# Kernel tuning notes

Measured on AMD Instinct MI355X. Metric: run time of the kernel, lower is better.

Reference implementation:

```python
import jax, jax.numpy as jnp
import numpy as np

B = 131072   # batch
D = 64       # latent_dim
P = 32       # n_pairs
H = 64       # hidden_dim
EMA = 1.0    # ema buffer initial value (detached in original, so a constant)


def setup_inputs() -> dict:
    key = jax.random.key(0)
    ks = jax.random.split(key, 4)
    z = jax.random.normal(ks[0], (B, D), dtype=jnp.float32)
    # tiny MLP params (2 -> H -> H -> 1), small init so exp(score) stays finite
    W1 = jax.random.normal(ks[1], (2, H), dtype=jnp.float32) * 0.05
    b1 = jnp.zeros((H,), jnp.float32)
    W2 = jax.random.normal(ks[2], (H, H), dtype=jnp.float32) * 0.05
    b2 = jnp.zeros((H,), jnp.float32)
    W3 = jax.random.normal(ks[3], (H, 1), dtype=jnp.float32) * 0.05
    b3 = jnp.zeros((1,), jnp.float32)
    # sampled dimension pairs: randperm(D)[:2] sorted, per pair
    rng = np.random.default_rng(0)
    idx = np.argsort(rng.random((P, D)), axis=1)[:, :2]
    pairs = jnp.asarray(np.sort(idx, axis=1).astype(np.int32))
    # per-pair batch permutations (randperm(B))
    perms = jnp.asarray(np.argsort(rng.random((P, B)), axis=1).astype(np.int32))
    return {"z": z, "W1": W1, "b1": b1, "W2": W2, "b2": b2,
            "W3": W3, "b3": b3, "pairs": pairs, "perms": perms}


def _mlp(x, W1, b1, W2, b2, W3, b3):
    # x: [P, B, 2] -> scores [P, B]
    h = jax.nn.elu(x @ W1 + b1)
    h = jax.nn.elu(h @ W2 + b2)
    return (h @ W3 + b3)[..., 0]


def reference(z, W1, b1, W2, b2, W3, b3, pairs, perms):
    # gather latent dims for all pairs at once: [P, B]
    z_i = z[:, pairs[:, 0]].T
    z_j = z[:, pairs[:, 1]].T
    z_i_sh = jnp.take_along_axis(z_i, perms, axis=1)  # shuffled marginals
    joint_in = jnp.stack([z_i, z_j], axis=-1)      # [P, B, 2]
    marg_in = jnp.stack([z_i_sh, z_j], axis=-1)    # [P, B, 2]
    joint = _mlp(joint_in, W1, b1, W2, b2, W3, b3)  # [P, B]
    marg = _mlp(marg_in, W1, b1, W2, b2, W3, b3)    # [P, B]
    et = jnp.mean(jnp.exp(marg), axis=1)            # [P]
    mi = jnp.mean(joint, axis=1) - jnp.log(et / EMA)
    return jnp.mean(mi)
```

## Files before the change

kernel.cpp:

```cpp
#include <hip/hip_runtime.h>
#include <hip/hip_bf16.h>
#include <math.h>

#define B_N   131072
#define D_DIM 64
#define P_N   32
#define H_DIM 64
#define TPB   256
#define GRIDX 64
#define SPB   (B_N / GRIDX)
#define SPI   128
#define ITERS (SPB / SPI)

#define K_L2E 1.44269504088896340736f
#define LN2F  0.693147180559945309f

typedef __attribute__((ext_vector_type(8))) short bf16x8;
typedef __attribute__((ext_vector_type(4))) float f32x4;

static __device__ __forceinline__ unsigned short bfbits(float f) {
    __hip_bfloat16 b = __float2bfloat16(f);
    unsigned short u; __builtin_memcpy(&u, &b, 2); return u;
}
static __device__ __forceinline__ float bf2f(unsigned short u) {
    return __uint_as_float(((unsigned)u) << 16);
}

__global__ void transpose_z(const float* __restrict__ z, float* __restrict__ zT) {
    __shared__ float tile[64][65];
    const int s0 = blockIdx.x * 64;
    const int t  = threadIdx.x;
    #pragma unroll
    for (int it = 0; it < 4; ++it) {
        int r  = it * 16 + (t >> 4);
        int c4 = (t & 15) * 4;
        const float4 v = *(const float4*)&z[(long)(s0 + r) * 64 + c4];
        tile[r][c4 + 0] = v.x; tile[r][c4 + 1] = v.y;
        tile[r][c4 + 2] = v.z; tile[r][c4 + 3] = v.w;
    }
    __syncthreads();
    #pragma unroll
    for (int it = 0; it < 16; ++it) {
        int d = it * 4 + (t >> 6);
        int s = t & 63;
        zT[d * B_N + s0 + s] = tile[s][d];
    }
}

__global__ void prep_weights(const float* __restrict__ W2,
                             unsigned short* __restrict__ w2hi,
                             unsigned short* __restrict__ w2lo) {
    int t = blockIdx.x * blockDim.x + threadIdx.x;
    int m = t & 7, l = (t >> 3) & 63, n = (t >> 9) & 3, c = t >> 11;
    int k = c * 32 + (l >> 4) * 8 + m;
    int col = n * 16 + (l & 15);
    float v = W2[k * 64 + col];
    unsigned short hi = bfbits(v);
    unsigned short lo = bfbits(v - bf2f(hi));
    w2hi[t] = hi;
    w2lo[t] = lo;
}

static __device__ __forceinline__ float eluK(float xk) {
    float e = __builtin_amdgcn_exp2f(xk);
    float neg = fmaf(e, K_L2E, -K_L2E);
    return xk > 0.0f ? xk : neg;
}

union Frag { unsigned u[4]; bf16x8 v; };

template<int ET, int TR>
__global__ __launch_bounds__(TPB, 2)
void mine_mfma(const float* __restrict__ zp,
               const float* __restrict__ W1, const float* __restrict__ b1,
               const unsigned short* __restrict__ w2hi,
               const unsigned short* __restrict__ w2lo,
               const float* __restrict__ b2,
               const float* __restrict__ W3,
               const int* __restrict__ pairs, const int* __restrict__ perms,
               double* __restrict__ partials) {
    const int wg = blockIdx.x;
    const int lg = (wg & 7) * (P_N * GRIDX / 8) + (wg >> 3);
    const int p  = lg >> 6;
    const int bx = lg & (GRIDX - 1);

    const int i    = pairs[2 * p];
    const int j    = pairs[2 * p + 1];
    const int tid  = threadIdx.x;
    const int lane = tid & 63;
    const int wv   = tid >> 6;
    const int g    = lane >> 4;
    const int r16  = lane & 15;

    #define ZA(idx) (TR ? zp[(long)i * B_N + (idx)] : zp[(long)(idx) * 64 + i])
    #define ZB(idx) (TR ? zp[(long)j * B_N + (idx)] : zp[(long)(idx) * 64 + j])

    float w1a[2][8], w1b[2][8], b1v[2][8];
    #pragma unroll
    for (int c = 0; c < 2; ++c)
        #pragma unroll
        for (int m = 0; m < 8; ++m) {
            int d = c * 32 + g * 8 + m;
            w1a[c][m] = W1[d]      * K_L2E;
            w1b[c][m] = W1[64 + d] * K_L2E;
            b1v[c][m] = b1[d]      * K_L2E;
        }

    const bf16x8* fh = (const bf16x8*)w2hi;
    const bf16x8* fl = (const bf16x8*)w2lo;
    bf16x8 wh[2][4], wl[2][4];
    #pragma unroll
    for (int c = 0; c < 2; ++c)
        #pragma unroll
        for (int n = 0; n < 4; ++n) {
            wh[c][n] = fh[(c * 4 + n) * 64 + lane];
            wl[c][n] = fl[(c * 4 + n) * 64 + lane];
        }

    float b2v[4], w3v[4];
    #pragma unroll
    for (int n = 0; n < 4; ++n) {
        b2v[n] = b2[n * 16 + r16] * K_L2E;
        w3v[n] = W3[n * 16 + r16] * LN2F;
    }

    const int  sbase = bx * SPB + wv * 16 + r16;
    const long pbase = (long)p * B_N;
    #define SIDX(t, u) (sbase + (t) * SPI + (u) * 64)

    float aC[2], bC[2], aN[2], bN[2];
    int   pmN2[2];
    #pragma unroll
    for (int u = 0; u < 2; ++u) {
        const int s0 = SIDX(0, u);
        const int s1 = SIDX(1, u);
        int pm0 = ET ? perms[pbase + s0] : s0;
        int pm1 = ET ? perms[pbase + s1] : s1;
        bC[u] = ZB(s0);  aC[u] = ZA(pm0);
        bN[u] = ZB(s1);  aN[u] = ZA(pm1);
        pmN2[u] = ET ? perms[pbase + SIDX(2, u)] : SIDX(2, u);
    }

    double acd0 = 0.0, acd1 = 0.0;

    for (int t = 0; t < ITERS; ++t) {
        const int t2 = (t + 2 < ITERS) ? t + 2 : ITERS - 1;
        const int t3 = (t + 3 < ITERS) ? t + 3 : ITERS - 1;
        int   pmN3[2];
        float bN2[2], aN2[2];
        #pragma unroll
        for (int u = 0; u < 2; ++u) {
            pmN3[u] = ET ? perms[pbase + SIDX(t3, u)] : SIDX(t3, u);
            bN2[u]  = ZB(SIDX(t2, u));
            aN2[u]  = ZA(pmN2[u]);
        }

        Frag ah[2][2], al[2][2];
        #pragma unroll
        for (int u = 0; u < 2; ++u)
            #pragma unroll
            for (int c = 0; c < 2; ++c)
                #pragma unroll
                for (int w = 0; w < 4; ++w) {
                    float pe = fmaf(aC[u], w1a[c][2*w],   fmaf(bC[u], w1b[c][2*w],   b1v[c][2*w]));
                    float po = fmaf(aC[u], w1a[c][2*w+1], fmaf(bC[u], w1b[c][2*w+1], b1v[c][2*w+1]));
                    float he = eluK(pe);
                    float ho = eluK(po);
                    unsigned ue = __float_as_uint(he), uo = __float_as_uint(ho);
                    ah[u][c].u[w] = __builtin_amdgcn_perm(uo, ue, 0x07060302u);
                    float le = he - __uint_as_float(ue & 0xFFFF0000u);
                    float lf = ho - __uint_as_float(uo & 0xFFFF0000u);
                    al[u][c].u[w] = __builtin_amdgcn_perm(__float_as_uint(lf),
                                                          __float_as_uint(le), 0x07060302u);
                }

        f32x4 acc[2][4];
        #pragma unroll
        for (int u = 0; u < 2; ++u)
            #pragma unroll
            for (int n = 0; n < 4; ++n)
                acc[u][n] = (f32x4){b2v[n], b2v[n], b2v[n], b2v[n]};
        #pragma unroll
        for (int u = 0; u < 2; ++u)
            #pragma unroll
            for (int c = 0; c < 2; ++c) {
                #pragma unroll
                for (int n = 0; n < 4; ++n)
                    acc[u][n] = __builtin_amdgcn_mfma_f32_16x16x32_bf16(ah[u][c].v, wh[c][n], acc[u][n], 0, 0, 0);
                #pragma unroll
                for (int n = 0; n < 4; ++n)
                    acc[u][n] = __builtin_amdgcn_mfma_f32_16x16x32_bf16(ah[u][c].v, wl[c][n], acc[u][n], 0, 0, 0);
                #pragma unroll
                for (int n = 0; n < 4; ++n)
                    acc[u][n] = __builtin_amdgcn_mfma_f32_16x16x32_bf16(al[u][c].v, wh[c][n], acc[u][n], 0, 0, 0);
            }

        float sc[2][4];
        #pragma unroll
        for (int u = 0; u < 2; ++u) {
            sc[u][0] = sc[u][1] = sc[u][2] = sc[u][3] = 0.f;
            #pragma unroll
            for (int r = 0; r < 4; ++r)
                #pragma unroll
                for (int n = 0; n < 4; ++n)
                    sc[u][r] = fmaf(eluK(acc[u][n][r]), w3v[n], sc[u][r]);
        }

        if (ET == 0) {
            acd0 += (double)((sc[0][0] + sc[0][1]) + (sc[0][2] + sc[0][3]));
            acd1 += (double)((sc[1][0] + sc[1][1]) + (sc[1][2] + sc[1][3]));
        } else {
            #pragma unroll
            for (int u = 0; u < 2; ++u) {
                const bool o1 = lane & 1;
                float k01 = o1 ? sc[u][1] : sc[u][0];
                float s01 = o1 ? sc[u][0] : sc[u][1];
                float v01 = k01 + __shfl_xor(s01, 1, 64);
                float k23 = o1 ? sc[u][3] : sc[u][2];
                float s23 = o1 ? sc[u][2] : sc[u][3];
                float v23 = k23 + __shfl_xor(s23, 1, 64);
                const bool o2 = lane & 2;
                float kk = o2 ? v23 : v01;
                float ss = o2 ? v01 : v23;
                float v  = kk + __shfl_xor(ss, 2, 64);
                v += __shfl_xor(v, 4, 64);
                v += __shfl_xor(v, 8, 64);
                if (u == 0) acd0 += (double)expf(v);
                else        acd1 += (double)expf(v);
            }
        }

        #pragma unroll
        for (int u = 0; u < 2; ++u) {
            aC[u] = aN[u]; bC[u] = bN[u];
            aN[u] = aN2[u]; bN[u] = bN2[u];
            pmN2[u] = pmN3[u];
        }
    }

    double accd = acd0 + acd1;

    __shared__ double red[TPB];
    red[tid] = accd;
    __syncthreads();
    for (int s = TPB / 2; s > 0; s >>= 1) {
        if (tid < s) red[tid] += red[tid + s];
        __syncthreads();
    }
    if (tid == 0) {
        double v = (ET == 0) ? red[0] : red[0] * 0.25;
        partials[ET * (P_N * GRIDX) + p * GRIDX + bx] = v;
    }
    #undef ZA
    #undef ZB
    #undef SIDX
}

__global__ void mine_final(const double* __restrict__ partials, float* __restrict__ out) {
    int lane = threadIdx.x;
    double mi = 0.0;
    if (lane < P_N) {
        double sj = 0.0, sm = 0.0;
        for (int c = 0; c < GRIDX; ++c) {
            sj += partials[lane * GRIDX + c];
            sm += partials[P_N * GRIDX + lane * GRIDX + c];
        }
        mi = sj / (double)B_N - log(sm / (double)B_N);
    }
    #pragma unroll
    for (int off = 32; off > 0; off >>= 1) mi += __shfl_down(mi, off);
    if (lane == 0) out[0] = (float)(mi / (double)P_N);
}

extern "C" void kernel_launch(void* const* d_in, const int* in_sizes, int n_in,
                              void* d_out, int out_size, void* d_ws, size_t ws_size,
                              hipStream_t stream) {
    const float* z     = (const float*)d_in[0];
    const float* W1    = (const float*)d_in[1];
    const float* b1    = (const float*)d_in[2];
    const float* W2    = (const float*)d_in[3];
    const float* b2    = (const float*)d_in[4];
    const float* W3    = (const float*)d_in[5];
    const int*   pairs = (const int*)d_in[7];
    const int*   perms = (const int*)d_in[8];

    const size_t ZT_BYTES = (size_t)D_DIM * B_N * sizeof(float);
    const bool   tr = ws_size >= ZT_BYTES + 65536;

    float* zT   = (float*)d_ws;
    char*  wb   = (char*)d_ws + (tr ? ZT_BYTES : 0);
    unsigned short* w2hi = (unsigned short*)wb;
    unsigned short* w2lo = (unsigned short*)(wb + 8192);
    double* partials     = (double*)(wb + 16384);

    prep_weights<<<16, 256, 0, stream>>>(W2, w2hi, w2lo);

    dim3 grid(P_N * GRIDX, 1, 1);
    if (tr) {
        transpose_z<<<B_N / 64, 256, 0, stream>>>(z, zT);
        mine_mfma<0, 1><<<grid, TPB, 0, stream>>>(zT, W1, b1, w2hi, w2lo, b2, W3,
                                                  pairs, perms, partials);
        mine_mfma<1, 1><<<grid, TPB, 0, stream>>>(zT, W1, b1, w2hi, w2lo, b2, W3,
                                                  pairs, perms, partials);
    } else {
        mine_mfma<0, 0><<<grid, TPB, 0, stream>>>(z, W1, b1, w2hi, w2lo, b2, W3,
                                                  pairs, perms, partials);
        mine_mfma<1, 0><<<grid, TPB, 0, stream>>>(z, W1, b1, w2hi, w2lo, b2, W3,
                                                  pairs, perms, partials);
    }
    mine_final<<<1, 64, 0, stream>>>(partials, (float*)d_out);
}
```

Measured before the change: 307.5 us.

## Fuse joint and marginal MLP passes into one kernel sharing z_j loads

Replaces the two separate kernel launches (joint and marginal) with one fused kernel. Each thread now evaluates the joint and shuffled-marginal inputs for the same sample, so the z_j value is loaded once and used by both paths, and SPI is halved to keep the same per-iteration work. This saves a launch and some redundant z_j reads, and the two sums are reduced one after the other in the epilogue. The cost is a longer single kernel and two block reductions per block.

```diff
diff --git a/kernel.cpp b/kernel.cpp
--- a/kernel.cpp
+++ b/kernel.cpp
@@ -9,7 +9,7 @@
 #define TPB   256
 #define GRIDX 64
 #define SPB   (B_N / GRIDX)
-#define SPI   128
+#define SPI   64
 #define ITERS (SPB / SPI)
 
 #define K_L2E 1.44269504088896340736f
@@ -69,16 +69,16 @@
 
 union Frag { unsigned u[4]; bf16x8 v; };
 
-template<int ET, int TR>
+template<int TR>
 __global__ __launch_bounds__(TPB, 2)
-void mine_mfma(const float* __restrict__ zp,
-               const float* __restrict__ W1, const float* __restrict__ b1,
-               const unsigned short* __restrict__ w2hi,
-               const unsigned short* __restrict__ w2lo,
-               const float* __restrict__ b2,
-               const float* __restrict__ W3,
-               const int* __restrict__ pairs, const int* __restrict__ perms,
-               double* __restrict__ partials) {
+void mine_fused(const float* __restrict__ zp,
+                const float* __restrict__ W1, const float* __restrict__ b1,
+                const unsigned short* __restrict__ w2hi,
+                const unsigned short* __restrict__ w2lo,
+                const float* __restrict__ b2,
+                const float* __restrict__ W3,
+                const int* __restrict__ pairs, const int* __restrict__ perms,
+                double* __restrict__ partials) {
     const int wg = blockIdx.x;
     const int lg = (wg & 7) * (P_N * GRIDX / 8) + (wg >> 3);
     const int p  = lg >> 6;
@@ -126,34 +126,32 @@
 
     const int  sbase = bx * SPB + wv * 16 + r16;
     const long pbase = (long)p * B_N;
-    #define SIDX(t, u) (sbase + (t) * SPI + (u) * 64)
-
-    float aC[2], bC[2], aN[2], bN[2];
-    int   pmN2[2];
-    #pragma unroll
-    for (int u = 0; u < 2; ++u) {
-        const int s0 = SIDX(0, u);
-        const int s1 = SIDX(1, u);
-        int pm0 = ET ? perms[pbase + s0] : s0;
-        int pm1 = ET ? perms[pbase + s1] : s1;
-        bC[u] = ZB(s0);  aC[u] = ZA(pm0);
-        bN[u] = ZB(s1);  aN[u] = ZA(pm1);
-        pmN2[u] = ET ? perms[pbase + SIDX(2, u)] : SIDX(2, u);
-    }
-
-    double acd0 = 0.0, acd1 = 0.0;
+    #define SIDX(t) (sbase + (t) * SPI)
+
+    float bC, bN;
+    float aC[2], aN[2];
+    int   pmN2;
+    {
+        const int s0 = SIDX(0);
+        const int s1 = SIDX(1);
+        int pm0 = perms[pbase + s0];
+        int pm1 = perms[pbase + s1];
+        bC = ZB(s0);  aC[0] = ZA(s0);  aC[1] = ZA(pm0);
+        bN = ZB(s1);  aN[0] = ZA(s1);  aN[1] = ZA(pm1);
+        pmN2 = perms[pbase + SIDX(2)];
+    }
+
+    double acdJ = 0.0, acdM = 0.0;
 
     for (int t = 0; t < ITERS; ++t) {
         const int t2 = (t + 2 < ITERS) ? t + 2 : ITERS - 1;
         const int t3 = (t + 3 < ITERS) ? t + 3 : ITERS - 1;
-        int   pmN3[2];
-        float bN2[2], aN2[2];
-        #pragma unroll
-        for (int u = 0; u < 2; ++u) {
-            pmN3[u] = ET ? perms[pbase + SIDX(t3, u)] : SIDX(t3, u);
-            bN2[u]  = ZB(SIDX(t2, u));
-            aN2[u]  = ZA(pmN2[u]);
-        }
+        const int sN2 = SIDX(t2);
+        int   pmN3 = perms[pbase + SIDX(t3)];
+        float bN2  = ZB(sN2);
+        float aN2[2];
+        aN2[0] = ZA(sN2);
+        aN2[1] = ZA(pmN2);
 
         Frag ah[2][2], al[2][2];
         #pragma unroll
@@ -162,8 +160,8 @@
             for (int c = 0; c < 2; ++c)
                 #pragma unroll
                 for (int w = 0; w < 4; ++w) {
-                    float pe = fmaf(aC[u], w1a[c][2*w],   fmaf(bC[u], w1b[c][2*w],   b1v[c][2*w]));
-                    float po = fmaf(aC[u], w1a[c][2*w+1], fmaf(bC[u], w1b[c][2*w+1], b1v[c][2*w+1]));
+                    float pe = fmaf(aC[u], w1a[c][2*w],   fmaf(bC, w1b[c][2*w],   b1v[c][2*w]));
+                    float po = fmaf(aC[u], w1a[c][2*w+1], fmaf(bC, w1b[c][2*w+1], b1v[c][2*w+1]));
                     float he = eluK(pe);
                     float ho = eluK(po);
                     unsigned ue = __float_as_uint(he), uo = __float_as_uint(ho);
@@ -206,51 +204,48 @@
                     sc[u][r] = fmaf(eluK(acc[u][n][r]), w3v[n], sc[u][r]);
         }
 
-        if (ET == 0) {
-            acd0 += (double)((sc[0][0] + sc[0][1]) + (sc[0][2] + sc[0][3]));
-            acd1 += (double)((sc[1][0] + sc[1][1]) + (sc[1][2] + sc[1][3]));
-        } else {
-            #pragma unroll
-            for (int u = 0; u < 2; ++u) {
-                const bool o1 = lane & 1;
-                float k01 = o1 ? sc[u][1] : sc[u][0];
-                float s01 = o1 ? sc[u][0] : sc[u][1];
-                float v01 = k01 + __shfl_xor(s01, 1, 64);
-                float k23 = o1 ? sc[u][3] : sc[u][2];
-                float s23 = o1 ? sc[u][2] : sc[u][3];
-                float v23 = k23 + __shfl_xor(s23, 1, 64);
-                const bool o2 = lane & 2;
-                float kk = o2 ? v23 : v01;
-                float ss = o2 ? v01 : v23;
-                float v  = kk + __shfl_xor(ss, 2, 64);
-                v += __shfl_xor(v, 4, 64);
-                v += __shfl_xor(v, 8, 64);
-                if (u == 0) acd0 += (double)expf(v);
-                else        acd1 += (double)expf(v);
-            }
-        }
-
-        #pragma unroll
-        for (int u = 0; u < 2; ++u) {
-            aC[u] = aN[u]; bC[u] = bN[u];
-            aN[u] = aN2[u]; bN[u] = bN2[u];
-            pmN2[u] = pmN3[u];
-        }
-    }
-
-    double accd = acd0 + acd1;
+        acdJ += (double)((sc[0][0] + sc[0][1]) + (sc[0][2] + sc[0][3]));
+
+        {
+            const bool o1 = lane & 1;
+            float k01 = o1 ? sc[1][1] : sc[1][0];
+            float s01 = o1 ? sc[1][0] : sc[1][1];
+            float v01 = k01 + __shfl_xor(s01, 1, 64);
+            float k23 = o1 ? sc[1][3] : sc[1][2];
+            float s23 = o1 ? sc[1][2] : sc[1][3];
+            float v23 = k23 + __shfl_xor(s23, 1, 64);
+            const bool o2 = lane & 2;
+            float kk = o2 ? v23 : v01;
+            float ss = o2 ? v01 : v23;
+            float v  = kk + __shfl_xor(ss, 2, 64);
+            v += __shfl_xor(v, 4, 64);
+            v += __shfl_xor(v, 8, 64);
+            acdM += (double)expf(v);
+        }
+
+        aC[0] = aN[0]; aC[1] = aN[1]; bC = bN;
+        aN[0] = aN2[0]; aN[1] = aN2[1]; bN = bN2;
+        pmN2 = pmN3;
+    }
 
     __shared__ double red[TPB];
-    red[tid] = accd;
+    red[tid] = acdJ;
     __syncthreads();
     for (int s = TPB / 2; s > 0; s >>= 1) {
         if (tid < s) red[tid] += red[tid + s];
         __syncthreads();
     }
-    if (tid == 0) {
-        double v = (ET == 0) ? red[0] : red[0] * 0.25;
-        partials[ET * (P_N * GRIDX) + p * GRIDX + bx] = v;
-    }
+    if (tid == 0)
+        partials[p * GRIDX + bx] = red[0];
+    __syncthreads();
+    red[tid] = acdM;
+    __syncthreads();
+    for (int s = TPB / 2; s > 0; s >>= 1) {
+        if (tid < s) red[tid] += red[tid + s];
+        __syncthreads();
+    }
+    if (tid == 0)
+        partials[P_N * GRIDX + p * GRIDX + bx] = red[0] * 0.25;
     #undef ZA
     #undef ZB
     #undef SIDX
@@ -298,15 +293,11 @@
     dim3 grid(P_N * GRIDX, 1, 1);
     if (tr) {
         transpose_z<<<B_N / 64, 256, 0, stream>>>(z, zT);
-        mine_mfma<0, 1><<<grid, TPB, 0, stream>>>(zT, W1, b1, w2hi, w2lo, b2, W3,
-                                                  pairs, perms, partials);
-        mine_mfma<1, 1><<<grid, TPB, 0, stream>>>(zT, W1, b1, w2hi, w2lo, b2, W3,
-                                                  pairs, perms, partials);
+        mine_fused<1><<<grid, TPB, 0, stream>>>(zT, W1, b1, w2hi, w2lo, b2, W3,
+                                                pairs, perms, partials);
     } else {
-        mine_mfma<0, 0><<<grid, TPB, 0, stream>>>(z, W1, b1, w2hi, w2lo, b2, W3,
-                                                  pairs, perms, partials);
-        mine_mfma<1, 0><<<grid, TPB, 0, stream>>>(z, W1, b1, w2hi, w2lo, b2, W3,
-                                                  pairs, perms, partials);
+        mine_fused<0><<<grid, TPB, 0, stream>>>(z, W1, b1, w2hi, w2lo, b2, W3,
+                                                pairs, perms, partials);
     }
     mine_final<<<1, 64, 0, stream>>>(partials, (float*)d_out);
 }
```

After: 316.8 us. 1.03x slower.
